# Performance work log

Hardware: AMD Instinct MI355X
Metric: run time of the kernel (lower is better)

Reference implementation:

```python
import jax, jax.numpy as jnp
import numpy as np

SUBSET_CHANNELS = 128


def setup_inputs() -> dict:
    key = jax.random.key(0)
    k_in, k_q, k_k, k_v = jax.random.split(key, 4)
    B, S, C, D = 8, 2048, 1024, SUBSET_CHANNELS
    scale = 1.0 / np.sqrt(C)  # ~ default torch Linear init scale
    return {
        "input": jax.random.normal(k_in, (B, S, C), dtype=jnp.float32),
        "Wq": jax.random.normal(k_q, (C, D), dtype=jnp.float32) * scale,
        "Wk": jax.random.normal(k_k, (C, D), dtype=jnp.float32) * scale,
        "Wv": jax.random.normal(k_v, (C, D), dtype=jnp.float32) * scale,
    }


def reference(input, Wq, Wk, Wv):
    # Projections (bias=False): [B,S,C] @ [C,D] -> [B,S,D]
    Q = input @ Wq
    K = input @ Wk
    V = input @ Wv
    D = Wq.shape[1]
    # scores[b, i, j] = Q[b,i,:] . K[b,j,:], scaled by sqrt(subset_channels)
    scores = jnp.einsum("bqd,bkd->bqk", Q, K) / jnp.sqrt(jnp.asarray(D, Q.dtype))
    # NOTE: original applies softmax over dim=1 (the QUERY axis), non-standard.
    att = jax.nn.softmax(scores, axis=1)
    # output[b, i, :] = sum_j att[b,i,j] * V[b,j,:]
    return jnp.einsum("bqk,bkd->bqd", att, V)
```

## Files before the change

### kernel.cpp

```cpp
#include <hip/hip_runtime.h>
#include <hip/hip_bf16.h>

typedef __bf16 bf16_t;
typedef bf16_t bf16x4 __attribute__((ext_vector_type(4)));
typedef bf16_t bf16x8 __attribute__((ext_vector_type(8)));
typedef float f32x4 __attribute__((ext_vector_type(4)));
typedef __attribute__((address_space(1))) const unsigned int gu32_t;
typedef __attribute__((address_space(3))) unsigned int lu32_t;

#define MFMA(a, b, c) __builtin_amdgcn_mfma_f32_16x16x32_bf16(a, b, c, 0, 0, 0)

constexpr int B = 8, S = 2048, C = 1024, D = 128;
constexpr float C2 = 0.12751744f;


__global__ __launch_bounds__(256) void k_wt(const float* Wq, const float* Wk, const float* Wv, bf16_t* Wf) {
    int ct = blockIdx.x, w = blockIdx.y;
    const float* src = (w == 0) ? Wq : ((w == 1) ? Wk : Wv);
    __shared__ bf16_t tile[16][132];
    int t = threadIdx.x;
    int cr = t >> 4, dq = t & 15;
    const float* p = src + (size_t)(ct * 16 + cr) * D + dq * 8;
    f32x4 v0 = *(const f32x4*)p;
    f32x4 v1 = *(const f32x4*)(p + 4);
#pragma unroll
    for (int q = 0; q < 4; ++q) { tile[cr][dq * 8 + q] = (bf16_t)v0[q]; tile[cr][dq * 8 + 4 + q] = (bf16_t)v1[q]; }
    __syncthreads();
    int n = t >> 1, g = t & 1;
    bf16x8 o;
#pragma unroll
    for (int cc = 0; cc < 8; ++cc) o[cc] = tile[g * 8 + cc][n];
    int c8 = ct * 2 + g;
    int nblk = w * 8 + (n >> 4);
    size_t a = ((size_t)(nblk * 32 + (c8 >> 2)) * 64 + (c8 & 3) * 16 + (n & 15)) * 8;
    *(bf16x8*)(Wf + a) = o;
}

__global__ __launch_bounds__(512) void k_qkv(const float* X, const bf16_t* Wf,
                                             bf16_t* Qf, bf16_t* Kf, float* Vf) {
    __shared__ __align__(16) bf16_t xs[2][4096];
    int mt = blockIdx.x;
    int t = threadIdx.x;
    int lane = t & 63, wid = t >> 6;
    int lr = lane & 15, lg = lane >> 4;
    int rw = mt * 64;
    int xrow = t >> 3, xk = t & 7;
    const float* xsrc = X + (size_t)(rw + xrow) * C + xk * 8;
    int xwi = ((xrow >> 4) * 8 + xk) * 128 + (xrow & 15) * 8;

    f32x4 acc[4][3] = {};

    {
        f32x4 x0 = *(const f32x4*)xsrc;
        f32x4 x1 = *(const f32x4*)(xsrc + 4);
        bf16x8 xv;
#pragma unroll
        for (int q = 0; q < 4; ++q) { xv[q] = (bf16_t)x0[q]; xv[4 + q] = (bf16_t)x1[q]; }
        *(bf16x8*)&xs[0][xwi] = xv;
    }
    __syncthreads();

    for (int tt = 0; tt < 16; ++tt) {
        int buf = tt & 1;
        bf16x8 w0[3], w1[3];
#pragma unroll
        for (int nf = 0; nf < 3; ++nf) {
            w0[nf] = *(const bf16x8*)(Wf + ((size_t)((wid * 3 + nf) * 32 + tt * 2) * 64 + lane) * 8);
            w1[nf] = *(const bf16x8*)(Wf + ((size_t)((wid * 3 + nf) * 32 + tt * 2 + 1) * 64 + lane) * 8);
        }
        f32x4 xp0, xp1;
        if (tt < 15) {
            xp0 = *(const f32x4*)(xsrc + (tt + 1) * 64);
            xp1 = *(const f32x4*)(xsrc + (tt + 1) * 64 + 4);
        }
#pragma unroll
        for (int rF = 0; rF < 4; ++rF) {
            bf16x8 a0 = *(bf16x8*)&xs[buf][(rF * 8 + lg) * 128 + lr * 8];
            bf16x8 a1 = *(bf16x8*)&xs[buf][(rF * 8 + 4 + lg) * 128 + lr * 8];
#pragma unroll
            for (int nf = 0; nf < 3; ++nf) {
                acc[rF][nf] = MFMA(a0, w0[nf], acc[rF][nf]);
                acc[rF][nf] = MFMA(a1, w1[nf], acc[rF][nf]);
            }
        }
        if (tt < 15) {
            bf16x8 xv;
#pragma unroll
            for (int q = 0; q < 4; ++q) { xv[q] = (bf16_t)xp0[q]; xv[4 + q] = (bf16_t)xp1[q]; }
            *(bf16x8*)&xs[buf ^ 1][xwi] = xv;
        }
        __syncthreads();
    }
#pragma unroll
    for (int rF = 0; rF < 4; ++rF)
#pragma unroll
        for (int nf = 0; nf < 3; ++nf) {
            int n = wid * 48 + nf * 16 + lr;
            int sel = (wid * 48 + nf * 16) >> 7;
            int nn = n & 127;
#pragma unroll
            for (int r = 0; r < 4; ++r) {
                int m = rw + rF * 16 + lg * 4 + r;
                float v = acc[rF][nf][r];
                if (sel == 2) {
                    Vf[(size_t)m * D + nn] = v;
                } else {
                    bf16_t* dst = (sel == 0) ? Qf : Kf;
                    size_t a = ((size_t)((m >> 4) * 4 + (nn >> 5)) * 64 + ((nn >> 3) & 3) * 16 + (m & 15)) * 8 + (nn & 7);
                    dst[a] = (bf16_t)v;
                }
            }
        }
}

__global__ __launch_bounds__(512) void k_sum(const bf16_t* Qf, const bf16_t* Kf,
                                             const float* Vf, bf16_t* Vt2) {
    int l = blockIdx.x;
    int b = l & 7, jt = l >> 3;
    int j0 = jt * 64;
    int t = threadIdx.x;
    int lane = t & 63, wid = t >> 6;
    int lr = lane & 15;
    __shared__ __align__(16) bf16_t qs[2][16384];
    bf16_t* vtile = qs[0];
    float* lsum = (float*)(qs[0] + 8192);
    float* linv = (float*)(qs[0] + 9216);

    bf16x8 kf[4][4];
    int jblkg = (b * S + j0) >> 4;
#pragma unroll
    for (int jF = 0; jF < 4; ++jF)
#pragma unroll
        for (int kk = 0; kk < 4; ++kk)
            kf[jF][kk] = *(const bf16x8*)(Kf + ((size_t)((jblkg + jF) * 4 + kk) * 64 + lane) * 8);

    const bf16_t* qsrc = Qf + (size_t)(b * S) * 128;
    auto stageQ = [&](int bufi, int i0) {
#pragma unroll
        for (int i = 0; i < 4; ++i)
            __builtin_amdgcn_global_load_lds(
                (gu32_t*)(qsrc + (size_t)i0 * 128 + wid * 2048 + i * 512 + lane * 8),
                (lu32_t*)&qs[bufi][wid * 2048 + i * 512], 16, 0, 0);
    };

    float ls[4] = {0.f, 0.f, 0.f, 0.f};
    stageQ(0, 0);
    __syncthreads();
    for (int tt = 0; tt < 16; ++tt) {
        int buf = tt & 1;
        if (tt < 15) stageQ(buf ^ 1, (tt + 1) * 128);
        bf16x8 qa[4];
#pragma unroll
        for (int kk = 0; kk < 4; ++kk)
            qa[kk] = *(const bf16x8*)&qs[buf][(wid * 4 + kk) * 512 + lane * 8];
        f32x4 s[4] = {};
#pragma unroll
        for (int kk = 0; kk < 4; ++kk) {
            s[0] = MFMA(qa[kk], kf[0][kk], s[0]);
            s[1] = MFMA(qa[kk], kf[1][kk], s[1]);
            s[2] = MFMA(qa[kk], kf[2][kk], s[2]);
            s[3] = MFMA(qa[kk], kf[3][kk], s[3]);
        }
#pragma unroll
        for (int jF = 0; jF < 4; ++jF)
#pragma unroll
            for (int r = 0; r < 4; ++r) ls[jF] += exp2f(s[jF][r] * C2);
        __syncthreads();
    }
#pragma unroll
    for (int jF = 0; jF < 4; ++jF) {
        float v = ls[jF];
        v += __shfl_xor(v, 16); v += __shfl_xor(v, 32);
        if (lane < 16) lsum[wid * 64 + jF * 16 + lane] = v;
    }
    __syncthreads();
    if (t < 64) {
        float ss = 0.f;
#pragma unroll
        for (int w = 0; w < 8; ++w) ss += lsum[w * 64 + t];
        linv[t] = 1.0f / ss;
    }
    __syncthreads();
#pragma unroll
    for (int p = 0; p < 4; ++p) {
        int u = p * 512 + t;
        int jj = u >> 5, dq = u & 31;
        f32x4 v = *(const f32x4*)(Vf + (size_t)(b * S + j0 + jj) * D + dq * 4);
        float inv = linv[jj];
        int colx = jj ^ ((dq & 7) << 3);
#pragma unroll
        for (int q = 0; q < 4; ++q)
            vtile[(dq * 4 + q) * 64 + colx] = (bf16_t)(v[q] * inv);
    }
    __syncthreads();
#pragma unroll
    for (int p = 0; p < 2; ++p) {
        int u = p * 512 + t;
        int d = u >> 3, jg = u & 7;
        int colx = (jg * 8) ^ (((d >> 2) & 7) << 3);
        bf16x8 row = *(const bf16x8*)&vtile[d * 64 + colx];
        size_t j32g = (size_t)b * 64 + (j0 >> 5) + (jg >> 2);
        size_t a = ((j32g * 8 + (d >> 4)) * 64 + (jg & 3) * 16 + (d & 15)) * 8;
        *(bf16x8*)(Vt2 + a) = row;
    }
}

__global__ __launch_bounds__(512) void k_out(const bf16_t* Qf, const bf16_t* Kf,
                                             const bf16_t* Vt2, float* Out) {
    int l = blockIdx.x;
    int b = l & 7, it = (l >> 3) & 15, jh = l >> 7;
    int ibase = it * 128;
    int t = threadIdx.x;
    int lane = t & 63, wid = t >> 6;
    int lr = lane & 15, lg = lane >> 4;
    int ig = wid >> 1, jq = wid & 1;
    __shared__ __align__(16) bf16_t pool[26624];
    bf16_t* klds = pool;
    bf16_t* pl = pool + 16384 + wid * 1280;

    bf16x8 qf[2][4];
    int iblkg = (b * S + ibase + ig * 32) >> 4;
#pragma unroll
    for (int iF = 0; iF < 2; ++iF)
#pragma unroll
        for (int kk = 0; kk < 4; ++kk)
            qf[iF][kk] = *(const bf16x8*)(Qf + ((size_t)((iblkg + iF) * 4 + kk) * 64 + lane) * 8);

    f32x4 acc[2][8] = {};
    const bf16_t* kbase = Kf + (size_t)(b * S + jh * 1024) * 128;
    const bf16_t* vbase = Vt2 + (size_t)b * D * S;

    auto stageK = [&](int bufi, int tt) {
        const bf16_t* g = kbase + (size_t)tt * 8192 + wid * 1024 + lane * 8;
        __builtin_amdgcn_global_load_lds((gu32_t*)g, (lu32_t*)&klds[bufi * 8192 + wid * 1024], 16, 0, 0);
        __builtin_amdgcn_global_load_lds((gu32_t*)(g + 512), (lu32_t*)&klds[bufi * 8192 + wid * 1024 + 512], 16, 0, 0);
    };
    stageK(0, 0);
    __syncthreads();

    for (int tt = 0; tt < 16; ++tt) {
        int buf = tt & 1;
        if (tt < 15) stageK(buf ^ 1, tt + 1);
        int j32 = jh * 32 + tt * 2 + jq;
        bf16x8 vv[8];
#pragma unroll
        for (int dc = 0; dc < 8; ++dc)
            vv[dc] = *(const bf16x8*)(vbase + ((size_t)(j32 * 8 + dc) * 64 + lane) * 8);
#pragma unroll
        for (int jF = 0; jF < 2; ++jF) {
            bf16x8 ka[4];
#pragma unroll
            for (int kk = 0; kk < 4; ++kk)
                ka[kk] = *(const bf16x8*)&klds[buf * 8192 + ((jq * 2 + jF) * 4 + kk) * 512 + lane * 8];
#pragma unroll
            for (int iF = 0; iF < 2; ++iF) {
                f32x4 s = {};
                s = MFMA(ka[0], qf[iF][0], s);
                s = MFMA(ka[1], qf[iF][1], s);
                s = MFMA(ka[2], qf[iF][2], s);
                s = MFMA(ka[3], qf[iF][3], s);
                bf16x4 pv;
#pragma unroll
                for (int r = 0; r < 4; ++r) pv[r] = (bf16_t)exp2f(s[r] * C2);
                *(bf16x4*)&pl[(iF * 16 + lr) * 40 + jF * 16 + lg * 4] = pv;
            }
        }
        bf16x8 pa0 = *(const bf16x8*)&pl[lr * 40 + lg * 8];
        bf16x8 pa1 = *(const bf16x8*)&pl[(16 + lr) * 40 + lg * 8];
        __builtin_amdgcn_s_setprio(1);
#pragma unroll
        for (int dc = 0; dc < 8; ++dc) {
            acc[0][dc] = MFMA(pa0, vv[dc], acc[0][dc]);
            acc[1][dc] = MFMA(pa1, vv[dc], acc[1][dc]);
        }
        __builtin_amdgcn_s_setprio(0);
        __syncthreads();
    }

    float* R0 = (float*)pool;
    float* R1 = (float*)(pool + 8192);
    auto wrR = [&](float* R) {
#pragma unroll
        for (int iF = 0; iF < 2; ++iF)
#pragma unroll
            for (int dc = 0; dc < 8; ++dc)
#pragma unroll
                for (int r = 0; r < 4; ++r)
                    R[(iF * 16 + lg * 4 + r) * 128 + dc * 16 + lr] = acc[iF][dc][r];
    };
    auto adR = [&](float* R) {
#pragma unroll
        for (int iF = 0; iF < 2; ++iF)
#pragma unroll
            for (int dc = 0; dc < 8; ++dc)
#pragma unroll
                for (int r = 0; r < 4; ++r)
                    acc[iF][dc][r] += R[(iF * 16 + lg * 4 + r) * 128 + dc * 16 + lr];
    };
    if (jq == 1 && ig < 2) wrR(ig == 0 ? R0 : R1);
    __syncthreads();
    if (jq == 0 && ig < 2) adR(ig == 0 ? R0 : R1);
    __syncthreads();
    if (jq == 1 && ig >= 2) wrR(ig == 2 ? R0 : R1);
    __syncthreads();
    if (jq == 0 && ig >= 2) adR(ig == 2 ? R0 : R1);
    if (jq == 0) {
#pragma unroll
        for (int iF = 0; iF < 2; ++iF)
#pragma unroll
            for (int dc = 0; dc < 8; ++dc)
#pragma unroll
                for (int r = 0; r < 4; ++r)
                    atomicAdd(&Out[(size_t)(b * S + ibase + ig * 32 + iF * 16 + lg * 4 + r) * 128 + dc * 16 + lr],
                              acc[iF][dc][r]);
    }
}

extern "C" void kernel_launch(void* const* d_in, const int* in_sizes, int n_in,
                              void* d_out, int out_size, void* d_ws, size_t ws_size,
                              hipStream_t stream) {
    const float* X  = (const float*)d_in[0];
    const float* Wq = (const float*)d_in[1];
    const float* Wk = (const float*)d_in[2];
    const float* Wv = (const float*)d_in[3];
    char* ws = (char*)d_ws;
    bf16_t* Wf  = (bf16_t*)(ws);
    bf16_t* Qf  = (bf16_t*)(ws + (1ull << 20));
    bf16_t* Kf  = (bf16_t*)(ws + (5ull << 20));
    float*  Vf  = (float*)(ws + (9ull << 20));
    bf16_t* Vt2 = (bf16_t*)(ws + (17ull << 20));
    float* Out = (float*)d_out;

    hipMemsetAsync(d_out, 0, (size_t)out_size * sizeof(float), stream);
    k_wt<<<dim3(64, 3), dim3(256), 0, stream>>>(Wq, Wk, Wv, Wf);
    k_qkv<<<dim3(256), dim3(512), 0, stream>>>(X, Wf, Qf, Kf, Vf);
    k_sum<<<dim3(256), dim3(512), 0, stream>>>(Qf, Kf, Vf, Vt2);
    k_out<<<dim3(256), dim3(512), 0, stream>>>(Qf, Kf, Vt2, Out);
}
```

Measured before the change: 103.9 us.

## Halve per-block tiles and double grid across QKV, colsum and output kernels

Each of the three main kernels now handles half as many rows per block (32 rows in the projection, 32 key columns in the column-sum pass, 64 queries in the output pass) and launches twice as many blocks, with occupancy hints of 4 blocks per CU. The output kernel now stages V tiles into LDS through async global-to-LDS loads next to K, and its cross-wave reduction is simplified to a single LDS exchange. The projection kernel reworks its double buffering so weight fragments are prefetched a step ahead. The aim is to fill all 256 CUs with more waves and hide latency, at the cost of more total K/Q reloads, more atomics and more LDS per block.

```diff
diff --git a/kernel.cpp b/kernel.cpp
--- a/kernel.cpp
+++ b/kernel.cpp
@@ -36,63 +36,92 @@
     *(bf16x8*)(Wf + a) = o;
 }
 
-__global__ __launch_bounds__(512) void k_qkv(const float* X, const bf16_t* Wf,
-                                             bf16_t* Qf, bf16_t* Kf, float* Vf) {
-    __shared__ __align__(16) bf16_t xs[2][4096];
+__global__ __launch_bounds__(512, 4) void k_qkv(const float* X, const bf16_t* Wf,
+                                                bf16_t* Qf, bf16_t* Kf, float* Vf) {
+    __shared__ __align__(16) bf16_t xs[2][2048];
     int mt = blockIdx.x;
     int t = threadIdx.x;
     int lane = t & 63, wid = t >> 6;
     int lr = lane & 15, lg = lane >> 4;
-    int rw = mt * 64;
-    int xrow = t >> 3, xk = t & 7;
-    const float* xsrc = X + (size_t)(rw + xrow) * C + xk * 8;
-    int xwi = ((xrow >> 4) * 8 + xk) * 128 + (xrow & 15) * 8;
-
-    f32x4 acc[4][3] = {};
-
+    int rw = mt * 32;
+    int xrow = t >> 4, xk = t & 15;
+    const float* xsrc = X + (size_t)(rw + xrow) * C + xk * 4;
+    int xwi = ((xk >> 1) * 32 + xrow) * 8 + (xk & 1) * 4;
+
+    f32x4 acc[2][3] = {};
+
+    auto wfrag = [&](int nf, int kk32) {
+        return *(const bf16x8*)(Wf + ((size_t)((wid * 3 + nf) * 32 + kk32) * 64 + lane) * 8);
+    };
+
+    bf16x8 wA[2][3], wB[2][3];
+#pragma unroll
+    for (int kh = 0; kh < 2; ++kh)
+#pragma unroll
+        for (int nf = 0; nf < 3; ++nf) wA[kh][nf] = wfrag(nf, kh);
     {
-        f32x4 x0 = *(const f32x4*)xsrc;
-        f32x4 x1 = *(const f32x4*)(xsrc + 4);
-        bf16x8 xv;
-#pragma unroll
-        for (int q = 0; q < 4; ++q) { xv[q] = (bf16_t)x0[q]; xv[4 + q] = (bf16_t)x1[q]; }
-        *(bf16x8*)&xs[0][xwi] = xv;
-    }
-    __syncthreads();
-
-    for (int tt = 0; tt < 16; ++tt) {
-        int buf = tt & 1;
-        bf16x8 w0[3], w1[3];
-#pragma unroll
-        for (int nf = 0; nf < 3; ++nf) {
-            w0[nf] = *(const bf16x8*)(Wf + ((size_t)((wid * 3 + nf) * 32 + tt * 2) * 64 + lane) * 8);
-            w1[nf] = *(const bf16x8*)(Wf + ((size_t)((wid * 3 + nf) * 32 + tt * 2 + 1) * 64 + lane) * 8);
-        }
-        f32x4 xp0, xp1;
-        if (tt < 15) {
-            xp0 = *(const f32x4*)(xsrc + (tt + 1) * 64);
-            xp1 = *(const f32x4*)(xsrc + (tt + 1) * 64 + 4);
-        }
-#pragma unroll
-        for (int rF = 0; rF < 4; ++rF) {
-            bf16x8 a0 = *(bf16x8*)&xs[buf][(rF * 8 + lg) * 128 + lr * 8];
-            bf16x8 a1 = *(bf16x8*)&xs[buf][(rF * 8 + 4 + lg) * 128 + lr * 8];
-#pragma unroll
-            for (int nf = 0; nf < 3; ++nf) {
-                acc[rF][nf] = MFMA(a0, w0[nf], acc[rF][nf]);
-                acc[rF][nf] = MFMA(a1, w1[nf], acc[rF][nf]);
-            }
-        }
-        if (tt < 15) {
-            bf16x8 xv;
-#pragma unroll
-            for (int q = 0; q < 4; ++q) { xv[q] = (bf16_t)xp0[q]; xv[4 + q] = (bf16_t)xp1[q]; }
-            *(bf16x8*)&xs[buf ^ 1][xwi] = xv;
-        }
-        __syncthreads();
-    }
-#pragma unroll
-    for (int rF = 0; rF < 4; ++rF)
+        f32x4 x = *(const f32x4*)xsrc;
+        bf16x4 xv;
+#pragma unroll
+        for (int q = 0; q < 4; ++q) xv[q] = (bf16_t)x[q];
+        *(bf16x4*)&xs[0][xwi] = xv;
+    }
+    __syncthreads();
+
+    for (int tt = 0; tt < 16; tt += 2) {
+        {
+#pragma unroll
+            for (int kh = 0; kh < 2; ++kh)
+#pragma unroll
+                for (int nf = 0; nf < 3; ++nf) wB[kh][nf] = wfrag(nf, (tt + 1) * 2 + kh);
+            f32x4 xp = *(const f32x4*)(xsrc + (tt + 1) * 64);
+#pragma unroll
+            for (int kh = 0; kh < 2; ++kh) {
+                bf16x8 a0 = *(bf16x8*)&xs[0][((kh * 4 + lg) * 32 + lr) * 8];
+                bf16x8 a1 = *(bf16x8*)&xs[0][((kh * 4 + lg) * 32 + 16 + lr) * 8];
+#pragma unroll
+                for (int nf = 0; nf < 3; ++nf) {
+                    acc[0][nf] = MFMA(a0, wA[kh][nf], acc[0][nf]);
+                    acc[1][nf] = MFMA(a1, wA[kh][nf], acc[1][nf]);
+                }
+            }
+            bf16x4 xv;
+#pragma unroll
+            for (int q = 0; q < 4; ++q) xv[q] = (bf16_t)xp[q];
+            *(bf16x4*)&xs[1][xwi] = xv;
+            __syncthreads();
+        }
+        {
+            bool pf = (tt + 2) < 16;
+            f32x4 xq;
+            if (pf) {
+#pragma unroll
+                for (int kh = 0; kh < 2; ++kh)
+#pragma unroll
+                    for (int nf = 0; nf < 3; ++nf) wA[kh][nf] = wfrag(nf, (tt + 2) * 2 + kh);
+                xq = *(const f32x4*)(xsrc + (tt + 2) * 64);
+            }
+#pragma unroll
+            for (int kh = 0; kh < 2; ++kh) {
+                bf16x8 a0 = *(bf16x8*)&xs[1][((kh * 4 + lg) * 32 + lr) * 8];
+                bf16x8 a1 = *(bf16x8*)&xs[1][((kh * 4 + lg) * 32 + 16 + lr) * 8];
+#pragma unroll
+                for (int nf = 0; nf < 3; ++nf) {
+                    acc[0][nf] = MFMA(a0, wB[kh][nf], acc[0][nf]);
+                    acc[1][nf] = MFMA(a1, wB[kh][nf], acc[1][nf]);
+                }
+            }
+            if (pf) {
+                bf16x4 xv;
+#pragma unroll
+                for (int q = 0; q < 4; ++q) xv[q] = (bf16_t)xq[q];
+                *(bf16x4*)&xs[0][xwi] = xv;
+            }
+            __syncthreads();
+        }
+    }
+#pragma unroll
+    for (int mi = 0; mi < 2; ++mi)
 #pragma unroll
         for (int nf = 0; nf < 3; ++nf) {
             int n = wid * 48 + nf * 16 + lr;
@@ -100,8 +129,8 @@
             int nn = n & 127;
 #pragma unroll
             for (int r = 0; r < 4; ++r) {
-                int m = rw + rF * 16 + lg * 4 + r;
-                float v = acc[rF][nf][r];
+                int m = rw + mi * 16 + lg * 4 + r;
+                float v = acc[mi][nf][r];
                 if (sel == 2) {
                     Vf[(size_t)m * D + nn] = v;
                 } else {
@@ -113,23 +142,22 @@
         }
 }
 
-__global__ __launch_bounds__(512) void k_sum(const bf16_t* Qf, const bf16_t* Kf,
-                                             const float* Vf, bf16_t* Vt2) {
+__global__ __launch_bounds__(512, 4) void k_sum(const bf16_t* Qf, const bf16_t* Kf,
+                                                const float* Vf, bf16_t* Vt2) {
     int l = blockIdx.x;
     int b = l & 7, jt = l >> 3;
-    int j0 = jt * 64;
+    int j0 = jt * 32;
     int t = threadIdx.x;
     int lane = t & 63, wid = t >> 6;
-    int lr = lane & 15;
     __shared__ __align__(16) bf16_t qs[2][16384];
     bf16_t* vtile = qs[0];
-    float* lsum = (float*)(qs[0] + 8192);
-    float* linv = (float*)(qs[0] + 9216);
-
-    bf16x8 kf[4][4];
+    float* lsum = (float*)(qs[0] + 6144);
+    float* linv = (float*)(qs[0] + 6656);
+
+    bf16x8 kf[2][4];
     int jblkg = (b * S + j0) >> 4;
 #pragma unroll
-    for (int jF = 0; jF < 4; ++jF)
+    for (int jF = 0; jF < 2; ++jF)
 #pragma unroll
         for (int kk = 0; kk < 4; ++kk)
             kf[jF][kk] = *(const bf16x8*)(Kf + ((size_t)((jblkg + jF) * 4 + kk) * 64 + lane) * 8);
@@ -143,7 +171,7 @@
                 (lu32_t*)&qs[bufi][wid * 2048 + i * 512], 16, 0, 0);
     };
 
-    float ls[4] = {0.f, 0.f, 0.f, 0.f};
+    float ls0 = 0.f, ls1 = 0.f;
     stageQ(0, 0);
     __syncthreads();
     for (int tt = 0; tt < 16; ++tt) {
@@ -153,166 +181,126 @@
 #pragma unroll
         for (int kk = 0; kk < 4; ++kk)
             qa[kk] = *(const bf16x8*)&qs[buf][(wid * 4 + kk) * 512 + lane * 8];
-        f32x4 s[4] = {};
+        f32x4 s0 = {}, s1 = {};
 #pragma unroll
         for (int kk = 0; kk < 4; ++kk) {
-            s[0] = MFMA(qa[kk], kf[0][kk], s[0]);
-            s[1] = MFMA(qa[kk], kf[1][kk], s[1]);
-            s[2] = MFMA(qa[kk], kf[2][kk], s[2]);
-            s[3] = MFMA(qa[kk], kf[3][kk], s[3]);
-        }
-#pragma unroll
-        for (int jF = 0; jF < 4; ++jF)
-#pragma unroll
-            for (int r = 0; r < 4; ++r) ls[jF] += exp2f(s[jF][r] * C2);
+            s0 = MFMA(qa[kk], kf[0][kk], s0);
+            s1 = MFMA(qa[kk], kf[1][kk], s1);
+        }
+#pragma unroll
+        for (int r = 0; r < 4; ++r) { ls0 += exp2f(s0[r] * C2); ls1 += exp2f(s1[r] * C2); }
         __syncthreads();
     }
-#pragma unroll
-    for (int jF = 0; jF < 4; ++jF) {
-        float v = ls[jF];
-        v += __shfl_xor(v, 16); v += __shfl_xor(v, 32);
-        if (lane < 16) lsum[wid * 64 + jF * 16 + lane] = v;
-    }
-    __syncthreads();
-    if (t < 64) {
+    {
+        float v0 = ls0 + __shfl_xor(ls0, 16); v0 += __shfl_xor(v0, 32);
+        float v1 = ls1 + __shfl_xor(ls1, 16); v1 += __shfl_xor(v1, 32);
+        if (lane < 16) { lsum[wid * 32 + lane] = v0; lsum[wid * 32 + 16 + lane] = v1; }
+    }
+    __syncthreads();
+    if (t < 32) {
         float ss = 0.f;
 #pragma unroll
-        for (int w = 0; w < 8; ++w) ss += lsum[w * 64 + t];
+        for (int w = 0; w < 8; ++w) ss += lsum[w * 32 + t];
         linv[t] = 1.0f / ss;
     }
     __syncthreads();
 #pragma unroll
-    for (int p = 0; p < 4; ++p) {
+    for (int p = 0; p < 2; ++p) {
         int u = p * 512 + t;
-        int jj = u >> 5, dq = u & 31;
+        int jj = u & 31, dq = u >> 5;
         f32x4 v = *(const f32x4*)(Vf + (size_t)(b * S + j0 + jj) * D + dq * 4);
         float inv = linv[jj];
-        int colx = jj ^ ((dq & 7) << 3);
 #pragma unroll
         for (int q = 0; q < 4; ++q)
-            vtile[(dq * 4 + q) * 64 + colx] = (bf16_t)(v[q] * inv);
-    }
-    __syncthreads();
-#pragma unroll
-    for (int p = 0; p < 2; ++p) {
-        int u = p * 512 + t;
-        int d = u >> 3, jg = u & 7;
-        int colx = (jg * 8) ^ (((d >> 2) & 7) << 3);
-        bf16x8 row = *(const bf16x8*)&vtile[d * 64 + colx];
-        size_t j32g = (size_t)b * 64 + (j0 >> 5) + (jg >> 2);
-        size_t a = ((j32g * 8 + (d >> 4)) * 64 + (jg & 3) * 16 + (d & 15)) * 8;
+            vtile[(dq * 4 + q) * 40 + jj] = (bf16_t)(v[q] * inv);
+    }
+    __syncthreads();
+    {
+        int d = t >> 2, jg = t & 3;
+        bf16x8 row = *(const bf16x8*)&vtile[d * 40 + jg * 8];
+        size_t j32g = (size_t)b * 64 + jt;
+        size_t a = ((j32g * 8 + (d >> 4)) * 64 + jg * 16 + (d & 15)) * 8;
         *(bf16x8*)(Vt2 + a) = row;
     }
 }
 
-__global__ __launch_bounds__(512) void k_out(const bf16_t* Qf, const bf16_t* Kf,
-                                             const bf16_t* Vt2, float* Out) {
+__global__ __launch_bounds__(512, 4) void k_out(const bf16_t* Qf, const bf16_t* Kf,
+                                                const bf16_t* Vt2, float* Out) {
     int l = blockIdx.x;
-    int b = l & 7, it = (l >> 3) & 15, jh = l >> 7;
-    int ibase = it * 128;
+    int b = l & 7, it = (l >> 3) & 31, jh = l >> 8;
+    int ibase = it * 64;
     int t = threadIdx.x;
     int lane = t & 63, wid = t >> 6;
     int lr = lane & 15, lg = lane >> 4;
     int ig = wid >> 1, jq = wid & 1;
-    __shared__ __align__(16) bf16_t pool[26624];
+    __shared__ __align__(16) bf16_t pool[37888];
     bf16_t* klds = pool;
-    bf16_t* pl = pool + 16384 + wid * 1280;
-
-    bf16x8 qf[2][4];
-    int iblkg = (b * S + ibase + ig * 32) >> 4;
-#pragma unroll
-    for (int iF = 0; iF < 2; ++iF)
-#pragma unroll
-        for (int kk = 0; kk < 4; ++kk)
-            qf[iF][kk] = *(const bf16x8*)(Qf + ((size_t)((iblkg + iF) * 4 + kk) * 64 + lane) * 8);
-
-    f32x4 acc[2][8] = {};
-    const bf16_t* kbase = Kf + (size_t)(b * S + jh * 1024) * 128;
-    const bf16_t* vbase = Vt2 + (size_t)b * D * S;
-
-    auto stageK = [&](int bufi, int tt) {
-        const bf16_t* g = kbase + (size_t)tt * 8192 + wid * 1024 + lane * 8;
-        __builtin_amdgcn_global_load_lds((gu32_t*)g, (lu32_t*)&klds[bufi * 8192 + wid * 1024], 16, 0, 0);
-        __builtin_amdgcn_global_load_lds((gu32_t*)(g + 512), (lu32_t*)&klds[bufi * 8192 + wid * 1024 + 512], 16, 0, 0);
+    bf16_t* vlds = pool + 16384;
+    bf16_t* pl = pool + 32768 + wid * 640;
+
+    bf16x8 qf[4];
+    int iblk = (b * S + ibase + ig * 16) >> 4;
+#pragma unroll
+    for (int kk = 0; kk < 4; ++kk)
+        qf[kk] = *(const bf16x8*)(Qf + ((size_t)(iblk * 4 + kk) * 64 + lane) * 8);
+
+    f32x4 acc[8] = {};
+    const bf16_t* kbase = Kf + (size_t)(b * S + jh * 1024) * 128 + wid * 1024 + lane * 8;
+    const bf16_t* vbase = Vt2 + (size_t)(b * 64 + jh * 32) * 4096 + wid * 1024 + lane * 8;
+
+    auto stageKV = [&](int bufi, int tt) {
+        const bf16_t* gk = kbase + (size_t)tt * 8192;
+        __builtin_amdgcn_global_load_lds((gu32_t*)gk, (lu32_t*)&klds[bufi * 8192 + wid * 1024], 16, 0, 0);
+        __builtin_amdgcn_global_load_lds((gu32_t*)(gk + 512), (lu32_t*)&klds[bufi * 8192 + wid * 1024 + 512], 16, 0, 0);
+        const bf16_t* gv = vbase + (size_t)tt * 8192;
+        __builtin_amdgcn_global_load_lds((gu32_t*)gv, (lu32_t*)&vlds[bufi * 8192 + wid * 1024], 16, 0, 0);
+        __builtin_amdgcn_global_load_lds((gu32_t*)(gv + 512), (lu32_t*)&vlds[bufi * 8192 + wid * 1024 + 512], 16, 0, 0);
     };
-    stageK(0, 0);
+    stageKV(0, 0);
     __syncthreads();
 
     for (int tt = 0; tt < 16; ++tt) {
         int buf = tt & 1;
-        if (tt < 15) stageK(buf ^ 1, tt + 1);
-        int j32 = jh * 32 + tt * 2 + jq;
-        bf16x8 vv[8];
+        if (tt < 15) stageKV(buf ^ 1, tt + 1);
+#pragma unroll
+        for (int jF = 0; jF < 2; ++jF) {
+            const bf16_t* kl = &klds[buf * 8192 + ((jq * 2 + jF) * 4) * 512 + lane * 8];
+            f32x4 s = {};
+            s = MFMA(*(const bf16x8*)(kl), qf[0], s);
+            s = MFMA(*(const bf16x8*)(kl + 512), qf[1], s);
+            s = MFMA(*(const bf16x8*)(kl + 1024), qf[2], s);
+            s = MFMA(*(const bf16x8*)(kl + 1536), qf[3], s);
+            bf16x4 pv;
+#pragma unroll
+            for (int r = 0; r < 4; ++r) pv[r] = (bf16_t)exp2f(s[r] * C2);
+            *(bf16x4*)&pl[lr * 40 + jF * 16 + lg * 4] = pv;
+        }
+        bf16x8 pa = *(const bf16x8*)&pl[lr * 40 + lg * 8];
+        const bf16_t* vl = &vlds[buf * 8192 + jq * 4096 + lane * 8];
+        __builtin_amdgcn_s_setprio(1);
 #pragma unroll
         for (int dc = 0; dc < 8; ++dc)
-            vv[dc] = *(const bf16x8*)(vbase + ((size_t)(j32 * 8 + dc) * 64 + lane) * 8);
-#pragma unroll
-        for (int jF = 0; jF < 2; ++jF) {
-            bf16x8 ka[4];
-#pragma unroll
-            for (int kk = 0; kk < 4; ++kk)
-                ka[kk] = *(const bf16x8*)&klds[buf * 8192 + ((jq * 2 + jF) * 4 + kk) * 512 + lane * 8];
-#pragma unroll
-            for (int iF = 0; iF < 2; ++iF) {
-                f32x4 s = {};
-                s = MFMA(ka[0], qf[iF][0], s);
-                s = MFMA(ka[1], qf[iF][1], s);
-                s = MFMA(ka[2], qf[iF][2], s);
-                s = MFMA(ka[3], qf[iF][3], s);
-                bf16x4 pv;
-#pragma unroll
-                for (int r = 0; r < 4; ++r) pv[r] = (bf16_t)exp2f(s[r] * C2);
-                *(bf16x4*)&pl[(iF * 16 + lr) * 40 + jF * 16 + lg * 4] = pv;
-            }
-        }
-        bf16x8 pa0 = *(const bf16x8*)&pl[lr * 40 + lg * 8];
-        bf16x8 pa1 = *(const bf16x8*)&pl[(16 + lr) * 40 + lg * 8];
-        __builtin_amdgcn_s_setprio(1);
-#pragma unroll
-        for (int dc = 0; dc < 8; ++dc) {
-            acc[0][dc] = MFMA(pa0, vv[dc], acc[0][dc]);
-            acc[1][dc] = MFMA(pa1, vv[dc], acc[1][dc]);
-        }
+            acc[dc] = MFMA(pa, *(const bf16x8*)(vl + dc * 512), acc[dc]);
         __builtin_amdgcn_s_setprio(0);
         __syncthreads();
     }
 
-    float* R0 = (float*)pool;
-    float* R1 = (float*)(pool + 8192);
-    auto wrR = [&](float* R) {
-#pragma unroll
-        for (int iF = 0; iF < 2; ++iF)
-#pragma unroll
-            for (int dc = 0; dc < 8; ++dc)
-#pragma unroll
-                for (int r = 0; r < 4; ++r)
-                    R[(iF * 16 + lg * 4 + r) * 128 + dc * 16 + lr] = acc[iF][dc][r];
-    };
-    auto adR = [&](float* R) {
-#pragma unroll
-        for (int iF = 0; iF < 2; ++iF)
-#pragma unroll
-            for (int dc = 0; dc < 8; ++dc)
-#pragma unroll
-                for (int r = 0; r < 4; ++r)
-                    acc[iF][dc][r] += R[(iF * 16 + lg * 4 + r) * 128 + dc * 16 + lr];
-    };
-    if (jq == 1 && ig < 2) wrR(ig == 0 ? R0 : R1);
-    __syncthreads();
-    if (jq == 0 && ig < 2) adR(ig == 0 ? R0 : R1);
-    __syncthreads();
-    if (jq == 1 && ig >= 2) wrR(ig == 2 ? R0 : R1);
-    __syncthreads();
-    if (jq == 0 && ig >= 2) adR(ig == 2 ? R0 : R1);
+    float* R = (float*)pool + ig * 2048;
+    if (jq == 1) {
+#pragma unroll
+        for (int dc = 0; dc < 8; ++dc)
+#pragma unroll
+            for (int r = 0; r < 4; ++r)
+                R[(lg * 4 + r) * 128 + dc * 16 + lr] = acc[dc][r];
+    }
+    __syncthreads();
     if (jq == 0) {
 #pragma unroll
-        for (int iF = 0; iF < 2; ++iF)
-#pragma unroll
-            for (int dc = 0; dc < 8; ++dc)
-#pragma unroll
-                for (int r = 0; r < 4; ++r)
-                    atomicAdd(&Out[(size_t)(b * S + ibase + ig * 32 + iF * 16 + lg * 4 + r) * 128 + dc * 16 + lr],
-                              acc[iF][dc][r]);
+        for (int dc = 0; dc < 8; ++dc)
+#pragma unroll
+            for (int r = 0; r < 4; ++r)
+                atomicAdd(&Out[(size_t)(b * S + ibase + ig * 16 + lg * 4 + r) * 128 + dc * 16 + lr],
+                          acc[dc][r] + R[(lg * 4 + r) * 128 + dc * 16 + lr]);
     }
 }
 
@@ -333,7 +321,7 @@
 
     hipMemsetAsync(d_out, 0, (size_t)out_size * sizeof(float), stream);
     k_wt<<<dim3(64, 3), dim3(256), 0, stream>>>(Wq, Wk, Wv, Wf);
-    k_qkv<<<dim3(256), dim3(512), 0, stream>>>(X, Wf, Qf, Kf, Vf);
-    k_sum<<<dim3(256), dim3(512), 0, stream>>>(Qf, Kf, Vf, Vt2);
-    k_out<<<dim3(256), dim3(512), 0, stream>>>(Qf, Kf, Vt2, Out);
-}
+    k_qkv<<<dim3(512), dim3(512), 0, stream>>>(X, Wf, Qf, Kf, Vf);
+    k_sum<<<dim3(512), dim3(512), 0, stream>>>(Qf, Kf, Vf, Vt2);
+    k_out<<<dim3(512), dim3(512), 0, stream>>>(Qf, Kf, Vt2, Out);
+}
```

After: 88.63 us. -14.7%, faster.
